# Kernel optimization log

Hardware: AMD Instinct MI355X
Metric: run time of the kernel (lower is better)

## Reference

```python
import jax, jax.numpy as jnp
import numpy as np

N = 50000      # nodes
E = 800000     # edges (avg degree 16)
D = 64         # emb_dim
L = 5          # num_layer
X_DIM = 92     # atom feature dim (hardwired in module)
EA_DIM = 50    # edge feature dim (edge_dim=50)
BN_EPS = 1e-5


def setup_inputs() -> dict:
    key = jax.random.key(0)
    ks = jax.random.split(key, 12)
    s = 0.05
    return {
        "x": jax.random.normal(ks[0], (N, X_DIM), jnp.float32),
        "edge_index": jax.random.randint(ks[1], (2, E), 0, N, dtype=jnp.int64),
        "edge_attr": jax.random.normal(ks[2], (E, EA_DIM), jnp.float32),
        # atom encoder: Linear(92, D)
        "atom_W": jax.random.normal(ks[3], (X_DIM, D), jnp.float32) * s,
        "atom_b": jnp.zeros((D,), jnp.float32),
        # per-layer GINEConv edge lin: Linear(50, D)
        "edge_W": jax.random.normal(ks[4], (L, EA_DIM, D), jnp.float32) * s,
        "edge_b": jnp.zeros((L, D), jnp.float32),
        # per-layer GIN MLP: Linear(D,D) -> ReLU -> Linear(D,D)
        "mlp_W1": jax.random.normal(ks[5], (L, D, D), jnp.float32) * s,
        "mlp_b1": jnp.zeros((L, D), jnp.float32),
        "mlp_W2": jax.random.normal(ks[6], (L, D, D), jnp.float32) * s,
        "mlp_b2": jnp.zeros((L, D), jnp.float32),
        # learnable eps (train_eps=True, init 0)
        "eps": jnp.zeros((L,), jnp.float32),
        # batch norm affine params
        "bn_gamma": jnp.ones((L, D), jnp.float32),
        "bn_beta": jnp.zeros((L, D), jnp.float32),
    }


def reference(x, edge_index, edge_attr, atom_W, atom_b, edge_W, edge_b,
              mlp_W1, mlp_b1, mlp_W2, mlp_b2, eps, bn_gamma, bn_beta):
    # edge_index[0] = src (message source), edge_index[1] = dst (aggregation target)
    # (adj = SparseTensor(row=ei[0], col=ei[1]); conv uses adj.t() -> aggregate at ei[1])
    src, dst = edge_index[0], edge_index[1]
    h = x @ atom_W + atom_b  # [N, D] atom encoder
    for l in range(L):
        # GINEConv message: relu(x_j + lin(edge_attr)), summed at destination
        m = jax.nn.relu(h[src] + edge_attr @ edge_W[l] + edge_b[l])  # [E, D]
        agg = jax.ops.segment_sum(m, dst, num_segments=N)             # [N, D]
        z = (1.0 + eps[l]) * h + agg
        z = jax.nn.relu(z @ mlp_W1[l] + mlp_b1[l]) @ mlp_W2[l] + mlp_b2[l]
        # BatchNorm1d (batch statistics over nodes)
        mu = jnp.mean(z, axis=0)
        var = jnp.var(z, axis=0)
        z = bn_gamma[l] * (z - mu) * jax.lax.rsqrt(var + BN_EPS) + bn_beta[l]
        # relu on all but last layer (dropout inactive in eval); residual=False
        h = z if l == L - 1 else jax.nn.relu(z)
    return h  # JK='last'
```

## Files before the change

kernel.cpp:

```cpp
#include <hip/hip_runtime.h>


#define NN 50000
#define NE 800000
#define D 64
#define NL 5
#define XD 92
#define EAD 50
#define BN_EPS 1e-5f
#define NBLK ((NN + 255) / 256)
#define TILE_E 256

__global__ void k_prep(const float* __restrict__ atomW, const float* __restrict__ W1,
                       const float* __restrict__ W2, const float* __restrict__ eW,
                       float* __restrict__ atomWt, float* __restrict__ W1t,
                       float* __restrict__ W2t, float* __restrict__ eWt) {
  int tid = blockIdx.x * blockDim.x + threadIdx.x;
  int nt = gridDim.x * blockDim.x;
  for (int i = tid; i < XD * D; i += nt) {
    int k = i / D, d = i % D;
    atomWt[d * XD + k] = atomW[i];
  }
  for (int i = tid; i < NL * D * D; i += nt) {
    int l = i / (D * D), r = i % (D * D);
    int k = r / D, d = r % D;
    W1t[(l * D + d) * D + k] = W1[i];
    W2t[(l * D + d) * D + k] = W2[i];
  }
  for (int i = tid; i < NL * EAD * D; i += nt) {
    int l = i / (EAD * D), r = i % (EAD * D);
    int k = r / D, d = r % D;
    eWt[(l * D + d) * EAD + k] = eW[i];
  }
}

__global__ __launch_bounds__(256) void k_atom(const float* __restrict__ x,
    const float* __restrict__ Wt, const float* __restrict__ b,
    float* __restrict__ h) {
  int n = blockIdx.x * blockDim.x + threadIdx.x;
  if (n >= NN) return;
  const float* xp = x + (size_t)n * XD;
  float xr[XD];
#pragma unroll
  for (int k = 0; k < XD; k += 4) {
    float4 v = *reinterpret_cast<const float4*>(xp + k);
    xr[k] = v.x; xr[k + 1] = v.y; xr[k + 2] = v.z; xr[k + 3] = v.w;
  }
  float hr[D];
#pragma unroll
  for (int d = 0; d < D; ++d) {
    const float* wr = Wt + d * XD;
    float a0 = 0.f, a1 = 0.f, a2 = 0.f, a3 = 0.f;
#pragma unroll
    for (int k = 0; k < XD; k += 4) {
      a0 = fmaf(xr[k + 0], wr[k + 0], a0);
      a1 = fmaf(xr[k + 1], wr[k + 1], a1);
      a2 = fmaf(xr[k + 2], wr[k + 2], a2);
      a3 = fmaf(xr[k + 3], wr[k + 3], a3);
    }
    hr[d] = (a0 + a1) + (a2 + a3) + b[d];
  }
  float* hp = h + (size_t)n * D;
#pragma unroll
  for (int d = 0; d < D; d += 4)
    *reinterpret_cast<float4*>(hp + d) = make_float4(hr[d], hr[d+1], hr[d+2], hr[d+3]);
}

__global__ __launch_bounds__(256) void k_deg(const int* __restrict__ ei,
                                             int* __restrict__ deg) {
  int e = blockIdx.x * blockDim.x + threadIdx.x;
  if (e < NE) atomicAdd(&deg[ei[NE + e]], 1);
}

__global__ __launch_bounds__(256) void k_scan_a(const int* __restrict__ deg,
    int* __restrict__ lps, int* __restrict__ bsum) {
  __shared__ int s[256];
  int t = threadIdx.x;
  int i = blockIdx.x * 256 + t;
  int v = (i < NN) ? deg[i] : 0;
  s[t] = v;
  __syncthreads();
#pragma unroll
  for (int off = 1; off < 256; off <<= 1) {
    int xv = (t >= off) ? s[t - off] : 0;
    __syncthreads();
    s[t] += xv;
    __syncthreads();
  }
  if (i < NN) lps[i] = s[t] - v;
  if (t == 255) bsum[blockIdx.x] = s[255];
}

__global__ __launch_bounds__(256) void k_scan_b(const int* __restrict__ bsum,
                                                int* __restrict__ bpre) {
  __shared__ int s[256];
  int t = threadIdx.x;
  int v = (t < NBLK) ? bsum[t] : 0;
  s[t] = v;
  __syncthreads();
#pragma unroll
  for (int off = 1; off < 256; off <<= 1) {
    int xv = (t >= off) ? s[t - off] : 0;
    __syncthreads();
    s[t] += xv;
    __syncthreads();
  }
  bpre[t] = s[t] - v;
}

__global__ __launch_bounds__(256) void k_fill(const int* __restrict__ lps,
    const int* __restrict__ bpre, int* __restrict__ rowptr,
    int* __restrict__ cursor) {
  int i = blockIdx.x * blockDim.x + threadIdx.x;
  if (i < NN) {
    int v = lps[i] + bpre[i >> 8];
    rowptr[i] = v;
    cursor[i] = v;
  }
  if (i == 0) rowptr[NN] = NE;
}

__global__ __launch_bounds__(256) void k_scatter(const int* __restrict__ ei,
    int* __restrict__ cursor, int* __restrict__ esrc, int* __restrict__ eidl,
    int* __restrict__ dstp) {
  int e = blockIdx.x * blockDim.x + threadIdx.x;
  if (e >= NE) return;
  int dst = ei[NE + e];
  int p = atomicAdd(&cursor[dst], 1);
  esrc[p] = ei[e];
  eidl[p] = e;
  dstp[p] = dst;
}

__global__ __launch_bounds__(256) void k_edge(const float* __restrict__ h,
    const float* __restrict__ ea, const float* __restrict__ eWt,
    const float* __restrict__ eb, const int* __restrict__ esrc,
    const int* __restrict__ eidl, const int* __restrict__ dstp,
    int layer, float* __restrict__ agg) {
  __shared__ float msg[4][64 * 33];
  int tid = threadIdx.x;
  int lane = tid & 63;
  int w = tid >> 6;
  int slot = blockIdx.x * TILE_E + w * 64 + lane;

  int eid  = eidl[slot];
  int vsrc = esrc[slot];
  int vdst = dstp[slot];

  const float* ep = ea + (size_t)eid * EAD;
  float4 ear[13];
#pragma unroll
  for (int q = 0; q < 12; ++q)
    ear[q] = *reinterpret_cast<const float4*>(ep + 4 * q);
  {
    float2 t2 = *reinterpret_cast<const float2*>(ep + 48);
    ear[12] = make_float4(t2.x, t2.y, 0.f, 0.f);
  }

  const float* Wl = eWt + (size_t)layer * D * EAD;
  const float* bl = eb + (size_t)layer * D;
  float* mw = msg[w];
  int half = lane >> 5;
  int l31 = lane & 31;

#pragma unroll
  for (int c = 0; c < 2; ++c) {
#pragma unroll 2
    for (int dc = 0; dc < 32; ++dc) {
      int d = c * 32 + dc;
      const float* wr = Wl + d * EAD;
      float a0 = 0.f, a1 = 0.f, a2 = 0.f, a3 = 0.f;
#pragma unroll
      for (int q = 0; q < 12; ++q) {
        a0 = fmaf(ear[q].x, wr[4 * q + 0], a0);
        a1 = fmaf(ear[q].y, wr[4 * q + 1], a1);
        a2 = fmaf(ear[q].z, wr[4 * q + 2], a2);
        a3 = fmaf(ear[q].w, wr[4 * q + 3], a3);
      }
      a0 = fmaf(ear[12].x, wr[48], a0);
      a1 = fmaf(ear[12].y, wr[49], a1);
      mw[lane * 33 + dc] = (a0 + a1) + (a2 + a3) + bl[d];
    }
    float acc = 0.f;
    int cur = __shfl(vdst, half);
#pragma unroll 4
    for (int i = 0; i < 32; ++i) {
      int e = 2 * i + half;
      int dste = __shfl(vdst, e);
      int srce = __shfl(vsrc, e);
      if (dste != cur) {
        unsafeAtomicAdd(&agg[(size_t)cur * D + c * 32 + l31], acc);
        acc = 0.f;
        cur = dste;
      }
      float lin = mw[e * 33 + l31];
      float hv = h[(size_t)srce * D + c * 32 + l31];
      acc += fmaxf(hv + lin, 0.f);
    }
    unsafeAtomicAdd(&agg[(size_t)cur * D + c * 32 + l31], acc);
  }
}

__global__ __launch_bounds__(256) void k_mlp(const float* __restrict__ h,
    const float* __restrict__ W1t, const float* __restrict__ b1,
    const float* __restrict__ W2t, const float* __restrict__ b2,
    const float* __restrict__ eps, int layer, float* __restrict__ agg) {
  int n = blockIdx.x * blockDim.x + threadIdx.x;
  if (n >= NN) return;
  float ope = 1.f + eps[layer];
  const float* hp = h + (size_t)n * D;
  float* ap = agg + (size_t)n * D;
  float zr[D];
#pragma unroll
  for (int k = 0; k < D; k += 4) {
    float4 hv = *reinterpret_cast<const float4*>(hp + k);
    float4 av = *reinterpret_cast<const float4*>(ap + k);
    zr[k]   = fmaf(ope, hv.x, av.x);
    zr[k+1] = fmaf(ope, hv.y, av.y);
    zr[k+2] = fmaf(ope, hv.z, av.z);
    zr[k+3] = fmaf(ope, hv.w, av.w);
  }
  const float* W1l = W1t + (size_t)layer * D * D;
  const float* b1l = b1 + layer * D;
  float y[D];
#pragma unroll
  for (int d = 0; d < D; ++d) {
    const float* wr = W1l + d * D;
    float a0 = 0.f, a1 = 0.f, a2 = 0.f, a3 = 0.f;
#pragma unroll
    for (int k = 0; k < D; k += 4) {
      a0 = fmaf(zr[k + 0], wr[k + 0], a0);
      a1 = fmaf(zr[k + 1], wr[k + 1], a1);
      a2 = fmaf(zr[k + 2], wr[k + 2], a2);
      a3 = fmaf(zr[k + 3], wr[k + 3], a3);
    }
    y[d] = fmaxf((a0 + a1) + (a2 + a3) + b1l[d], 0.f);
  }
  const float* W2l = W2t + (size_t)layer * D * D;
  const float* b2l = b2 + layer * D;
#pragma unroll
  for (int d = 0; d < D; ++d) {
    const float* wr = W2l + d * D;
    float a0 = 0.f, a1 = 0.f, a2 = 0.f, a3 = 0.f;
#pragma unroll
    for (int k = 0; k < D; k += 4) {
      a0 = fmaf(y[k + 0], wr[k + 0], a0);
      a1 = fmaf(y[k + 1], wr[k + 1], a1);
      a2 = fmaf(y[k + 2], wr[k + 2], a2);
      a3 = fmaf(y[k + 3], wr[k + 3], a3);
    }
    zr[d] = (a0 + a1) + (a2 + a3) + b2l[d];
  }
#pragma unroll
  for (int d = 0; d < D; d += 4)
    *reinterpret_cast<float4*>(ap + d) = make_float4(zr[d], zr[d+1], zr[d+2], zr[d+3]);
}

__global__ __launch_bounds__(256) void k_stats(const float* __restrict__ t,
                                               float* __restrict__ stats) {
  int lane = threadIdx.x & 63;
  int w = threadIdx.x >> 6;
  int gw = blockIdx.x * 4 + w;
  int nw = gridDim.x * 4;
  float s = 0.f, q = 0.f;
  for (int n = gw; n < NN; n += nw) {
    float v = t[(size_t)n * D + lane];
    s += v;
    q = fmaf(v, v, q);
  }
  __shared__ float ls[8][64];
  ls[w][lane] = s;
  ls[4 + w][lane] = q;
  __syncthreads();
  if (threadIdx.x < D) {
    float S = ls[0][lane] + ls[1][lane] + ls[2][lane] + ls[3][lane];
    float Q = ls[4][lane] + ls[5][lane] + ls[6][lane] + ls[7][lane];
    unsafeAtomicAdd(&stats[lane], S);
    unsafeAtomicAdd(&stats[D + lane], Q);
  }
}

__global__ __launch_bounds__(256) void k_apply(const float* __restrict__ t,
    const float* __restrict__ stats, const float* __restrict__ gamma,
    const float* __restrict__ beta, int layer, int last, float* __restrict__ o) {
  const float inv = 1.f / (float)NN;
  int i = blockIdx.x * blockDim.x + threadIdx.x;
  int nt = gridDim.x * blockDim.x;
  for (; i < NN * D / 4; i += nt) {
    int d0 = (i & 15) * 4;
    float4 v = reinterpret_cast<const float4*>(t)[i];
    float vv[4] = {v.x, v.y, v.z, v.w};
    float r[4];
#pragma unroll
    for (int c = 0; c < 4; ++c) {
      int d = d0 + c;
      float mu = stats[d] * inv;
      float var = fmaf(-mu, mu, stats[D + d] * inv);
      float sc = gamma[layer * D + d] / sqrtf(var + BN_EPS);
      float val = fmaf(vv[c] - mu, sc, beta[layer * D + d]);
      r[c] = last ? val : fmaxf(val, 0.f);
    }
    reinterpret_cast<float4*>(o)[i] = make_float4(r[0], r[1], r[2], r[3]);
  }
}

extern "C" void kernel_launch(void* const* d_in, const int* in_sizes, int n_in,
                              void* d_out, int out_size, void* d_ws, size_t ws_size,
                              hipStream_t stream) {
  const float* x     = (const float*)d_in[0];
  const int*   ei    = (const int*)d_in[1];
  const float* ea    = (const float*)d_in[2];
  const float* atomW = (const float*)d_in[3];
  const float* atomB = (const float*)d_in[4];
  const float* eW    = (const float*)d_in[5];
  const float* eb    = (const float*)d_in[6];
  const float* W1    = (const float*)d_in[7];
  const float* b1    = (const float*)d_in[8];
  const float* W2    = (const float*)d_in[9];
  const float* b2    = (const float*)d_in[10];
  const float* eps   = (const float*)d_in[11];
  const float* gamma = (const float*)d_in[12];
  const float* beta  = (const float*)d_in[13];
  float* out = (float*)d_out;

  char* ws = (char*)d_ws;
  float* h      = (float*)ws;
  float* agg    = h + (size_t)NN * D;
  float* stats  = agg + (size_t)NN * D;
  float* atomWt = stats + 2 * D;
  float* W1t    = atomWt + D * XD;
  float* W2t    = W1t + NL * D * D;
  float* eWt    = W2t + NL * D * D;
  int*   deg    = (int*)(eWt + NL * D * EAD);
  int*   lps    = deg + NN;
  int*   rowptr = lps + NN;
  int*   cursor = rowptr + NN + 1;
  int*   bsum   = cursor + NN;
  int*   bpre   = bsum + 256;
  int*   esrc   = bpre + 256;
  int*   eidl   = esrc + NE;
  int*   dstp   = eidl + NE;

  k_prep<<<64, 256, 0, stream>>>(atomW, W1, W2, eW, atomWt, W1t, W2t, eWt);
  k_atom<<<(NN + 255) / 256, 256, 0, stream>>>(x, atomWt, atomB, h);

  hipMemsetAsync(deg, 0, (size_t)NN * 4, stream);
  k_deg<<<(NE + 255) / 256, 256, 0, stream>>>(ei, deg);
  k_scan_a<<<NBLK, 256, 0, stream>>>(deg, lps, bsum);
  k_scan_b<<<1, 256, 0, stream>>>(bsum, bpre);
  k_fill<<<NBLK, 256, 0, stream>>>(lps, bpre, rowptr, cursor);
  k_scatter<<<(NE + 255) / 256, 256, 0, stream>>>(ei, cursor, esrc, eidl, dstp);

  for (int l = 0; l < NL; ++l) {
    hipMemsetAsync(agg, 0, ((size_t)NN * D + 2 * D) * 4, stream);
    k_edge<<<NE / TILE_E, 256, 0, stream>>>(h, ea, eWt, eb, esrc, eidl, dstp, l, agg);
    k_mlp<<<NBLK, 256, 0, stream>>>(h, W1t, b1, W2t, b2, eps, l, agg);
    k_stats<<<512, 256, 0, stream>>>(agg, stats);
    float* ho = (l == NL - 1) ? out : h;
    k_apply<<<1024, 256, 0, stream>>>(agg, stats, gamma, beta, l, (l == NL - 1) ? 1 : 0, ho);
  }
}
```

Baseline: 2.221 ms.

## Map edge features per lane with register-resident weights; split MLP outputs across waves

The edge kernel now keeps one output channel per lane, holding that channel's column of the edge weights in registers. It walks the wave's 64 edges serially, broadcasting each edge's index with readlane and loading the edge attributes uniformly. This removes the LDS message buffer, the transposed weight copy and the shuffles, at the cost of 64 serial iterations of broadcast loads per wave. The MLP kernel now processes 64 nodes per block, with each of the 4 waves computing 16 output features. The hidden layer is exchanged through LDS, which cuts per-thread register use and raises occupancy but adds a barrier and recomputes the input load in every wave.

```diff
diff --git a/kernel.cpp b/kernel.cpp
--- a/kernel.cpp
+++ b/kernel.cpp
@@ -10,11 +10,11 @@
 #define BN_EPS 1e-5f
 #define NBLK ((NN + 255) / 256)
 #define TILE_E 256
+#define MLPB ((NN + 63) / 64)
 
 __global__ void k_prep(const float* __restrict__ atomW, const float* __restrict__ W1,
-                       const float* __restrict__ W2, const float* __restrict__ eW,
-                       float* __restrict__ atomWt, float* __restrict__ W1t,
-                       float* __restrict__ W2t, float* __restrict__ eWt) {
+                       const float* __restrict__ W2, float* __restrict__ atomWt,
+                       float* __restrict__ W1t, float* __restrict__ W2t) {
   int tid = blockIdx.x * blockDim.x + threadIdx.x;
   int nt = gridDim.x * blockDim.x;
   for (int i = tid; i < XD * D; i += nt) {
@@ -26,11 +26,6 @@
     int k = r / D, d = r % D;
     W1t[(l * D + d) * D + k] = W1[i];
     W2t[(l * D + d) * D + k] = W2[i];
-  }
-  for (int i = tid; i < NL * EAD * D; i += nt) {
-    int l = i / (EAD * D), r = i % (EAD * D);
-    int k = r / D, d = r % D;
-    eWt[(l * D + d) * EAD + k] = eW[i];
   }
 }
 
@@ -133,83 +128,76 @@
 }
 
 __global__ __launch_bounds__(256) void k_edge(const float* __restrict__ h,
-    const float* __restrict__ ea, const float* __restrict__ eWt,
+    const float* __restrict__ ea, const float* __restrict__ eW,
     const float* __restrict__ eb, const int* __restrict__ esrc,
     const int* __restrict__ eidl, const int* __restrict__ dstp,
     int layer, float* __restrict__ agg) {
-  __shared__ float msg[4][64 * 33];
   int tid = threadIdx.x;
   int lane = tid & 63;
   int w = tid >> 6;
-  int slot = blockIdx.x * TILE_E + w * 64 + lane;
-
-  int eid  = eidl[slot];
-  int vsrc = esrc[slot];
-  int vdst = dstp[slot];
-
-  const float* ep = ea + (size_t)eid * EAD;
-  float4 ear[13];
-#pragma unroll
-  for (int q = 0; q < 12; ++q)
-    ear[q] = *reinterpret_cast<const float4*>(ep + 4 * q);
-  {
-    float2 t2 = *reinterpret_cast<const float2*>(ep + 48);
-    ear[12] = make_float4(t2.x, t2.y, 0.f, 0.f);
-  }
-
-  const float* Wl = eWt + (size_t)layer * D * EAD;
-  const float* bl = eb + (size_t)layer * D;
-  float* mw = msg[w];
-  int half = lane >> 5;
-  int l31 = lane & 31;
-
-#pragma unroll
-  for (int c = 0; c < 2; ++c) {
+  int base = blockIdx.x * TILE_E + w * 64;
+
+  int veid = eidl[base + lane];
+  int vsrc = esrc[base + lane];
+  int vdst = dstp[base + lane];
+
+  const float* Wl = eW + (size_t)layer * EAD * D;
+  float wc[EAD];
+#pragma unroll
+  for (int k = 0; k < EAD; ++k) wc[k] = Wl[k * D + lane];
+  float bd = eb[layer * D + lane];
+
+  int zoff = 0;
+  asm volatile("" : "+v"(zoff));
+
+  float acc = 0.f;
+  int cur = __builtin_amdgcn_readlane(vdst, 0);
 #pragma unroll 2
-    for (int dc = 0; dc < 32; ++dc) {
-      int d = c * 32 + dc;
-      const float* wr = Wl + d * EAD;
-      float a0 = 0.f, a1 = 0.f, a2 = 0.f, a3 = 0.f;
-#pragma unroll
-      for (int q = 0; q < 12; ++q) {
-        a0 = fmaf(ear[q].x, wr[4 * q + 0], a0);
-        a1 = fmaf(ear[q].y, wr[4 * q + 1], a1);
-        a2 = fmaf(ear[q].z, wr[4 * q + 2], a2);
-        a3 = fmaf(ear[q].w, wr[4 * q + 3], a3);
-      }
-      a0 = fmaf(ear[12].x, wr[48], a0);
-      a1 = fmaf(ear[12].y, wr[49], a1);
-      mw[lane * 33 + dc] = (a0 + a1) + (a2 + a3) + bl[d];
-    }
-    float acc = 0.f;
-    int cur = __shfl(vdst, half);
-#pragma unroll 4
-    for (int i = 0; i < 32; ++i) {
-      int e = 2 * i + half;
-      int dste = __shfl(vdst, e);
-      int srce = __shfl(vsrc, e);
-      if (dste != cur) {
-        unsafeAtomicAdd(&agg[(size_t)cur * D + c * 32 + l31], acc);
-        acc = 0.f;
-        cur = dste;
-      }
-      float lin = mw[e * 33 + l31];
-      float hv = h[(size_t)srce * D + c * 32 + l31];
-      acc += fmaxf(hv + lin, 0.f);
-    }
-    unsafeAtomicAdd(&agg[(size_t)cur * D + c * 32 + l31], acc);
-  }
+  for (int j = 0; j < 64; ++j) {
+    int eid = __builtin_amdgcn_readlane(veid, j);
+    int src = __builtin_amdgcn_readlane(vsrc, j);
+    int dst = __builtin_amdgcn_readlane(vdst, j);
+    const float* ep = ea + (size_t)eid * EAD + zoff;
+    float2 er[25];
+#pragma unroll
+    for (int q = 0; q < 25; ++q)
+      er[q] = *reinterpret_cast<const float2*>(ep + 2 * q);
+    float hv = h[(size_t)src * D + lane];
+    if (dst != cur) {
+      unsafeAtomicAdd(&agg[(size_t)cur * D + lane], acc);
+      acc = 0.f;
+      cur = dst;
+    }
+    float a0 = 0.f, a1 = 0.f, a2 = 0.f, a3 = 0.f;
+#pragma unroll
+    for (int q = 0; q < 24; q += 2) {
+      a0 = fmaf(er[q].x, wc[2 * q + 0], a0);
+      a1 = fmaf(er[q].y, wc[2 * q + 1], a1);
+      a2 = fmaf(er[q + 1].x, wc[2 * q + 2], a2);
+      a3 = fmaf(er[q + 1].y, wc[2 * q + 3], a3);
+    }
+    a0 = fmaf(er[24].x, wc[48], a0);
+    a1 = fmaf(er[24].y, wc[49], a1);
+    float lin = (a0 + a1) + (a2 + a3) + bd;
+    acc += fmaxf(hv + lin, 0.f);
+  }
+  unsafeAtomicAdd(&agg[(size_t)cur * D + lane], acc);
 }
 
 __global__ __launch_bounds__(256) void k_mlp(const float* __restrict__ h,
     const float* __restrict__ W1t, const float* __restrict__ b1,
     const float* __restrict__ W2t, const float* __restrict__ b2,
     const float* __restrict__ eps, int layer, float* __restrict__ agg) {
-  int n = blockIdx.x * blockDim.x + threadIdx.x;
-  if (n >= NN) return;
+  __shared__ float ylds[64 * 68];
+  int tid = threadIdx.x;
+  int lane = tid & 63;
+  int w = tid >> 6;
+  int n = blockIdx.x * 64 + lane;
+  bool act = (n < NN);
+  int nc = act ? n : (NN - 1);
   float ope = 1.f + eps[layer];
-  const float* hp = h + (size_t)n * D;
-  float* ap = agg + (size_t)n * D;
+  const float* hp = h + (size_t)nc * D;
+  const float* ap = agg + (size_t)nc * D;
   float zr[D];
 #pragma unroll
   for (int k = 0; k < D; k += 4) {
@@ -221,10 +209,11 @@
     zr[k+3] = fmaf(ope, hv.w, av.w);
   }
   const float* W1l = W1t + (size_t)layer * D * D;
-  const float* b1l = b1 + layer * D;
-  float y[D];
-#pragma unroll
-  for (int d = 0; d < D; ++d) {
+  const float* b1p = b1 + layer * D;
+  float y[16];
+#pragma unroll
+  for (int dd = 0; dd < 16; ++dd) {
+    int d = w * 16 + dd;
     const float* wr = W1l + d * D;
     float a0 = 0.f, a1 = 0.f, a2 = 0.f, a3 = 0.f;
 #pragma unroll
@@ -234,26 +223,44 @@
       a2 = fmaf(zr[k + 2], wr[k + 2], a2);
       a3 = fmaf(zr[k + 3], wr[k + 3], a3);
     }
-    y[d] = fmaxf((a0 + a1) + (a2 + a3) + b1l[d], 0.f);
+    y[dd] = fmaxf((a0 + a1) + (a2 + a3) + b1p[d], 0.f);
+  }
+  float* yl = &ylds[lane * 68 + w * 16];
+#pragma unroll
+  for (int q = 0; q < 4; ++q)
+    *reinterpret_cast<float4*>(yl + 4 * q) =
+        make_float4(y[4*q], y[4*q+1], y[4*q+2], y[4*q+3]);
+  __syncthreads();
+  float yr[D];
+#pragma unroll
+  for (int q = 0; q < 16; ++q) {
+    float4 v = *reinterpret_cast<const float4*>(&ylds[lane * 68 + 4 * q]);
+    yr[4*q] = v.x; yr[4*q+1] = v.y; yr[4*q+2] = v.z; yr[4*q+3] = v.w;
   }
   const float* W2l = W2t + (size_t)layer * D * D;
-  const float* b2l = b2 + layer * D;
-#pragma unroll
-  for (int d = 0; d < D; ++d) {
+  const float* b2p = b2 + layer * D;
+  float tq[16];
+#pragma unroll
+  for (int dd = 0; dd < 16; ++dd) {
+    int d = w * 16 + dd;
     const float* wr = W2l + d * D;
     float a0 = 0.f, a1 = 0.f, a2 = 0.f, a3 = 0.f;
 #pragma unroll
     for (int k = 0; k < D; k += 4) {
-      a0 = fmaf(y[k + 0], wr[k + 0], a0);
-      a1 = fmaf(y[k + 1], wr[k + 1], a1);
-      a2 = fmaf(y[k + 2], wr[k + 2], a2);
-      a3 = fmaf(y[k + 3], wr[k + 3], a3);
-    }
-    zr[d] = (a0 + a1) + (a2 + a3) + b2l[d];
-  }
-#pragma unroll
-  for (int d = 0; d < D; d += 4)
-    *reinterpret_cast<float4*>(ap + d) = make_float4(zr[d], zr[d+1], zr[d+2], zr[d+3]);
+      a0 = fmaf(yr[k + 0], wr[k + 0], a0);
+      a1 = fmaf(yr[k + 1], wr[k + 1], a1);
+      a2 = fmaf(yr[k + 2], wr[k + 2], a2);
+      a3 = fmaf(yr[k + 3], wr[k + 3], a3);
+    }
+    tq[dd] = (a0 + a1) + (a2 + a3) + b2p[d];
+  }
+  if (act) {
+    float* op = agg + (size_t)n * D + w * 16;
+#pragma unroll
+    for (int q = 0; q < 4; ++q)
+      *reinterpret_cast<float4*>(op + 4 * q) =
+          make_float4(tq[4*q], tq[4*q+1], tq[4*q+2], tq[4*q+3]);
+  }
 }
 
 __global__ __launch_bounds__(256) void k_stats(const float* __restrict__ t,
@@ -330,8 +337,7 @@
   float* atomWt = stats + 2 * D;
   float* W1t    = atomWt + D * XD;
   float* W2t    = W1t + NL * D * D;
-  float* eWt    = W2t + NL * D * D;
-  int*   deg    = (int*)(eWt + NL * D * EAD);
+  int*   deg    = (int*)(W2t + NL * D * D);
   int*   lps    = deg + NN;
   int*   rowptr = lps + NN;
   int*   cursor = rowptr + NN + 1;
@@ -341,7 +347,7 @@
   int*   eidl   = esrc + NE;
   int*   dstp   = eidl + NE;
 
-  k_prep<<<64, 256, 0, stream>>>(atomW, W1, W2, eW, atomWt, W1t, W2t, eWt);
+  k_prep<<<64, 256, 0, stream>>>(atomW, W1, W2, atomWt, W1t, W2t);
   k_atom<<<(NN + 255) / 256, 256, 0, stream>>>(x, atomWt, atomB, h);
 
   hipMemsetAsync(deg, 0, (size_t)NN * 4, stream);
@@ -353,8 +359,8 @@
 
   for (int l = 0; l < NL; ++l) {
     hipMemsetAsync(agg, 0, ((size_t)NN * D + 2 * D) * 4, stream);
-    k_edge<<<NE / TILE_E, 256, 0, stream>>>(h, ea, eWt, eb, esrc, eidl, dstp, l, agg);
-    k_mlp<<<NBLK, 256, 0, stream>>>(h, W1t, b1, W2t, b2, eps, l, agg);
+    k_edge<<<NE / TILE_E, 256, 0, stream>>>(h, ea, eW, eb, esrc, eidl, dstp, l, agg);
+    k_mlp<<<MLPB, 256, 0, stream>>>(h, W1t, b1, W2t, b2, eps, l, agg);
     k_stats<<<512, 256, 0, stream>>>(agg, stats);
     float* ho = (l == NL - 1) ? out : h;
     k_apply<<<1024, 256, 0, stream>>>(agg, stats, gamma, beta, l, (l == NL - 1) ? 1 : 0, ho);
```

Result: slower. 2.709 ms (+22.0%).
